# Performance work log

Hardware: AMD Instinct MI355X
Metric: run time of the kernel (lower is better)

## Reference

```python
import jax, jax.numpy as jnp
import numpy as np

B, S, V, H = 64, 512, 128, 1024
TEMP = 1.0


def _lstm_layer(x_seq, W_ih, W_hh, b_ih, b_hh):
    """x_seq: (S, B, D_in) -> (S, B, H). PyTorch gate order: i, f, g, o."""
    Hh = W_hh.shape[1]
    Bb = x_seq.shape[1]
    # precompute input projections for all timesteps: (S, B, 4H)
    xW = jnp.einsum('sbd,gd->sbg', x_seq, W_ih) + (b_ih + b_hh)

    def step(carry, xw_t):
        h, c = carry
        gates = xw_t + h @ W_hh.T  # (B, 4H)
        i, f, g, o = jnp.split(gates, 4, axis=-1)
        i = jax.nn.sigmoid(i)
        f = jax.nn.sigmoid(f)
        g = jnp.tanh(g)
        o = jax.nn.sigmoid(o)
        c = f * c + i * g
        h = o * jnp.tanh(c)
        return (h, c), h

    h0 = jnp.zeros((Bb, Hh), dtype=x_seq.dtype)
    c0 = jnp.zeros((Bb, Hh), dtype=x_seq.dtype)
    _, hs = jax.lax.scan(step, (h0, c0), xW)
    return hs  # (S, B, H)


def setup_inputs() -> dict:
    key = jax.random.key(0)
    ks = jax.random.split(key, 11)
    s = 1.0 / np.sqrt(H)
    u = lambda k, shape: jax.random.uniform(k, shape, jnp.float32, -s, s)
    return {
        'x': jax.random.normal(ks[0], (B, S, V), jnp.float32),
        'W_ih0': u(ks[1], (4 * H, V)),
        'W_hh0': u(ks[2], (4 * H, H)),
        'b_ih0': u(ks[3], (4 * H,)),
        'b_hh0': u(ks[4], (4 * H,)),
        'W_ih1': u(ks[5], (4 * H, H)),
        'W_hh1': u(ks[6], (4 * H, H)),
        'b_ih1': u(ks[7], (4 * H,)),
        'b_hh1': u(ks[8], (4 * H,)),
        'W_fc': u(ks[9], (V, H)),
        'b_fc': u(ks[10], (V,)),
    }


def reference(x, W_ih0, W_hh0, b_ih0, b_hh0, W_ih1, W_hh1, b_ih1, b_hh1, W_fc, b_fc):
    xs = jnp.transpose(x, (1, 0, 2))  # (S, B, V)
    h1 = _lstm_layer(xs, W_ih0, W_hh0, b_ih0, b_hh0)   # (S, B, H)
    h2 = _lstm_layer(h1, W_ih1, W_hh1, b_ih1, b_hh1)   # (S, B, H)
    logits = jnp.einsum('sbh,vh->sbv', h2, W_fc) + b_fc  # (S, B, V)
    out = jax.nn.log_softmax(logits * TEMP, axis=-1)
    return jnp.transpose(out, (1, 0, 2))  # (B, S, V)
```

## Files before the change

kernel.cpp:

```cpp
#include <hip/hip_runtime.h>
#include <hip/hip_bf16.h>
#include <math.h>


#define S_LEN 512
#define B_SZ  64
#define V_SZ  128
#define H_SZ  1024
#define BH    65536
#define RING  8
#define FSTR  16

typedef unsigned short u16;
typedef unsigned short u16x8 __attribute__((ext_vector_type(8)));
typedef __bf16         bf16x8 __attribute__((ext_vector_type(8)));
typedef float          f32x4  __attribute__((ext_vector_type(4)));
typedef int            i32x4  __attribute__((ext_vector_type(4)));

__device__ __forceinline__ u16 f2bf(float f) {
    unsigned int u = __float_as_uint(f);
    u += 0x7fffu + ((u >> 16) & 1u);
    return (u16)(u >> 16);
}
__device__ __forceinline__ f32x4 mfma16(u16x8 a, u16x8 b, f32x4 c) {
    return __builtin_amdgcn_mfma_f32_16x16x32_bf16(
        __builtin_bit_cast(bf16x8, a), __builtin_bit_cast(bf16x8, b), c, 0, 0, 0);
}
__device__ __forceinline__ f32x4 mfma16(i32x4 a, u16x8 b, f32x4 c) {
    return __builtin_amdgcn_mfma_f32_16x16x32_bf16(
        __builtin_bit_cast(bf16x8, a), __builtin_bit_cast(bf16x8, b), c, 0, 0, 0);
}

__device__ __forceinline__ void ld_coh(i32x4& d, const u16* p) {
    asm volatile("global_load_dwordx4 %0, %1, off sc0 sc1" : "=v"(d) : "v"(p));
}
__device__ __forceinline__ void st_coh_u16(u16* p, u16 v) {
    unsigned int vv = v;
    asm volatile("global_store_short %0, %1, off sc0 sc1" :: "v"(p), "v"(vv));
}
__device__ __forceinline__ int ld_flag(const int* p) {
    int v;
    asm volatile("global_load_dword %0, %1, off sc0 sc1\n\ts_waitcnt vmcnt(0)"
                 : "=v"(v) : "v"(p) : "memory");
    return v;
}
__device__ __forceinline__ void st_flag(int* p, int v) {
    asm volatile("global_store_dword %0, %1, off sc0 sc1" :: "v"(p), "v"(v));
}
#define WAITV(n) asm volatile("s_waitcnt vmcnt(" #n ")" ::: "memory")
#define SCHEDB   __builtin_amdgcn_sched_barrier(0)

__global__ __launch_bounds__(256) void cvt_kernel(const float* __restrict__ s,
                                                  u16* __restrict__ d, int n)
{
    int i = (blockIdx.x * 256 + threadIdx.x) * 4;
    if (i >= n) return;
    float4 v = *(const float4*)(s + i);
    ushort4 o;
    o.x = f2bf(v.x); o.y = f2bf(v.y); o.z = f2bf(v.z); o.w = f2bf(v.w);
    *(ushort4*)(d + i) = o;
}

union SMemL {
    struct { u16 wih[64 * 136]; u16 whh[64 * 1032]; } l0;
    struct { u16 w[64 * 1032]; } l1;
    float lg[16][132];
};

__global__ __launch_bounds__(256, 1) void persist_kernel(
    const float* __restrict__ x,
    const u16* __restrict__ Wih0c, const u16* __restrict__ Whh0c,
    const u16* __restrict__ Wih1c, const u16* __restrict__ Whh1c,
    const u16* __restrict__ Wfcc,
    const float* __restrict__ bih0, const float* __restrict__ bhh0,
    const float* __restrict__ bih1, const float* __restrict__ bhh1,
    const float* __restrict__ bfc,
    u16* __restrict__ h0b, u16* __restrict__ h1b,
    int* __restrict__ flagL0, int* __restrict__ flagL1, int* __restrict__ flagFC,
    float* __restrict__ out)
{
    __shared__ SMemL sm;
    const int bid = blockIdx.x, tid = threadIdx.x;
    const int wave = tid >> 6, lane = tid & 63;
    const int l16 = lane & 15, kgi = lane >> 4, kg8 = kgi * 8;

    if (bid < 64) {
        const int j0 = bid * 16, jj = j0 + l16;
        for (int ch = tid; ch < 1024; ch += 256) {
            int rr = ch >> 4, kc = (ch & 15) * 8;
            int gr = (rr >> 4) * H_SZ + j0 + (rr & 15);
            *(u16x8*)&sm.l0.wih[rr * 136 + kc] = *(const u16x8*)(Wih0c + (size_t)gr * V_SZ + kc);
        }
        for (int ch = tid; ch < 8192; ch += 256) {
            int rr = ch >> 7, kc = (ch & 127) * 8;
            int gr = (rr >> 4) * H_SZ + j0 + (rr & 15);
            *(u16x8*)&sm.l0.whh[rr * 1032 + kc] = *(const u16x8*)(Whh0c + (size_t)gr * H_SZ + kc);
        }
        __syncthreads();

        const float bii = bih0[jj]            + bhh0[jj];
        const float bif = bih0[H_SZ + jj]     + bhh0[H_SZ + jj];
        const float big = bih0[2 * H_SZ + jj] + bhh0[2 * H_SZ + jj];
        const float bio = bih0[3 * H_SZ + jj] + bhh0[3 * H_SZ + jj];

        const u16* wihB[4]; const u16* whhB[4];
        #pragma unroll
        for (int g = 0; g < 4; ++g) {
            wihB[g] = &sm.l0.wih[(g * 16 + l16) * 136 + kg8];
            whhB[g] = &sm.l0.whh[(g * 16 + l16) * 1032 + kg8];
        }
        const int arow = wave * 16 + l16;
        const float* xrow = x + (size_t)arow * (S_LEN * V_SZ);
        float creg[4] = {0.f, 0.f, 0.f, 0.f};

        for (int t = 0; t < S_LEN; ++t) {
            {
                const int* p = nullptr; int tgt = 0;
                if (tid < 64)               { p = flagL0 + tid * FSTR;        tgt = t; }
                else if (tid < 192 && t >= 8) { p = flagL1 + (tid - 64) * FSTR; tgt = t - 7; }
                if (p && tgt > 0) while (ld_flag(p) < tgt) __builtin_amdgcn_s_sleep(2);
                __syncthreads();
            }

            f32x4 acc[4][2] = {};
            {
                const float* xp = xrow + (size_t)t * V_SZ + kg8;
                #pragma unroll
                for (int i = 0; i < 4; ++i) {
                    float4 u = *(const float4*)(xp + i * 32);
                    float4 v = *(const float4*)(xp + i * 32 + 4);
                    u16x8 af;
                    af[0] = f2bf(u.x); af[1] = f2bf(u.y); af[2] = f2bf(u.z); af[3] = f2bf(u.w);
                    af[4] = f2bf(v.x); af[5] = f2bf(v.y); af[6] = f2bf(v.z); af[7] = f2bf(v.w);
                    #pragma unroll
                    for (int g = 0; g < 4; ++g)
                        acc[g][i & 1] = mfma16(af, *(const u16x8*)(wihB[g] + i * 32), acc[g][i & 1]);
                }
            }

            {
                auto ISSUE = [&](i32x4 (&buf)[8], const u16* base) {
                    #pragma unroll
                    for (int q = 0; q < 8; ++q) ld_coh(buf[q], base + q * 32);
                };
                auto COMP = [&](i32x4 (&buf)[8], int k0) {
                    #pragma unroll
                    for (int q = 0; q < 8; ++q) {
                        #pragma unroll
                        for (int g = 0; g < 4; ++g)
                            acc[g][q & 1] = mfma16(buf[q],
                                *(const u16x8*)(whhB[g] + (k0 + q) * 32), acc[g][q & 1]);
                    }
                };
                const u16* aB = h0b + (size_t)((t - 1) & 7) * BH + (size_t)arow * H_SZ + kg8;
                i32x4 b0[8], b1[8];
                WAITV(0);
                ISSUE(b0, aB);
                ISSUE(b1, aB + 256); WAITV(8); SCHEDB; COMP(b0, 0);
                ISSUE(b0, aB + 512); WAITV(8); SCHEDB; COMP(b1, 8);
                ISSUE(b1, aB + 768); WAITV(8); SCHEDB; COMP(b0, 16);
                                     WAITV(0); SCHEDB; COMP(b1, 24);
            }

            {
                u16* hout = h0b + (size_t)(t & 7) * BH;
                #pragma unroll
                for (int r = 0; r < 4; ++r) {
                    const int m = wave * 16 + kgi * 4 + r;
                    const float ip = acc[0][0][r] + acc[0][1][r] + bii;
                    const float fp = acc[1][0][r] + acc[1][1][r] + bif;
                    const float gp = acc[2][0][r] + acc[2][1][r] + big;
                    const float op = acc[3][0][r] + acc[3][1][r] + bio;
                    const float iv = 1.f / (1.f + expf(-ip));
                    const float fv = 1.f / (1.f + expf(-fp));
                    const float gv = tanhf(gp);
                    const float ov = 1.f / (1.f + expf(-op));
                    const float cv = fv * creg[r] + iv * gv;
                    creg[r] = cv;
                    st_coh_u16(hout + (size_t)m * H_SZ + jj, f2bf(ov * tanhf(cv)));
                }
                WAITV(0);
            }
            __syncthreads();
            if (tid == 0) st_flag(flagL0 + bid * FSTR, t + 1);
        }
        return;
    }

    if (bid < 192) {
        const int lb = bid - 64, j0 = lb * 8, jj2 = j0 + (l16 & 7);
        for (int ch = tid; ch < 8192; ch += 256) {
            int region = ch >> 12;
            int rl = (ch >> 7) & 31, kc = (ch & 127) * 8;
            int gr = (rl >> 3) * H_SZ + j0 + (rl & 7);
            const u16* src = (region ? Whh1c : Wih1c) + (size_t)gr * H_SZ + kc;
            *(u16x8*)&sm.l1.w[(region * 32 + rl) * 1032 + kc] = *(const u16x8*)src;
        }
        __syncthreads();

        const float bii = bih1[jj2]            + bhh1[jj2];
        const float bif = bih1[H_SZ + jj2]     + bhh1[H_SZ + jj2];
        const float big = bih1[2 * H_SZ + jj2] + bhh1[2 * H_SZ + jj2];
        const float bio = bih1[3 * H_SZ + jj2] + bhh1[3 * H_SZ + jj2];
        const bool lo = (l16 < 8);

        const u16* wB1[2]; const u16* wB2[2];
        #pragma unroll
        for (int nt = 0; nt < 2; ++nt) {
            wB1[nt] = &sm.l1.w[(nt * 16 + l16) * 1032 + kg8];
            wB2[nt] = &sm.l1.w[(32 + nt * 16 + l16) * 1032 + kg8];
        }
        const int arow = wave * 16 + l16;
        float creg[4] = {0.f, 0.f, 0.f, 0.f};

        for (int t = 0; t < S_LEN; ++t) {
            {
                const int* p = nullptr; int tgt = 0;
                if (tid < 64)                     { p = flagL0 + tid * FSTR;         tgt = t + 1; }
                else if (tid < 192)               { p = flagL1 + (tid - 64) * FSTR;  tgt = t; }
                else if (tid < 196 && t >= 8)     { p = flagFC + (tid - 192) * FSTR; tgt = t - 7; }
                if (p && tgt > 0) while (ld_flag(p) < tgt) __builtin_amdgcn_s_sleep(2);
                __syncthreads();
            }

            f32x4 acc[2][2] = {};
            {
                auto ISSUE = [&](i32x4 (&buf)[8], const u16* base) {
                    #pragma unroll
                    for (int q = 0; q < 8; ++q) ld_coh(buf[q], base + q * 32);
                };
                auto COMP = [&](i32x4 (&buf)[8], const u16* const (&wb)[2], int k0) {
                    #pragma unroll
                    for (int q = 0; q < 8; ++q) {
                        #pragma unroll
                        for (int nt = 0; nt < 2; ++nt)
                            acc[nt][q & 1] = mfma16(buf[q],
                                *(const u16x8*)(wb[nt] + (k0 + q) * 32), acc[nt][q & 1]);
                    }
                };
                const u16* a1 = h0b + (size_t)(t & 7) * BH + (size_t)arow * H_SZ + kg8;
                const u16* a2 = h1b + (size_t)((t - 1) & 7) * BH + (size_t)arow * H_SZ + kg8;
                i32x4 b0[8], b1[8];
                WAITV(0);
                ISSUE(b0, a1);
                ISSUE(b1, a1 + 256); WAITV(8); SCHEDB; COMP(b0, wB1, 0);
                ISSUE(b0, a1 + 512); WAITV(8); SCHEDB; COMP(b1, wB1, 8);
                ISSUE(b1, a1 + 768); WAITV(8); SCHEDB; COMP(b0, wB1, 16);
                ISSUE(b0, a2);       WAITV(8); SCHEDB; COMP(b1, wB1, 24);
                ISSUE(b1, a2 + 256); WAITV(8); SCHEDB; COMP(b0, wB2, 0);
                ISSUE(b0, a2 + 512); WAITV(8); SCHEDB; COMP(b1, wB2, 8);
                ISSUE(b1, a2 + 768); WAITV(8); SCHEDB; COMP(b0, wB2, 16);
                                     WAITV(0); SCHEDB; COMP(b1, wB2, 24);
            }

            {
                u16* hout = h1b + (size_t)(t & 7) * BH;
                #pragma unroll
                for (int r = 0; r < 4; ++r) {
                    const float s0 = acc[0][0][r] + acc[0][1][r];
                    const float s1 = acc[1][0][r] + acc[1][1][r];
                    const float q0 = __shfl_xor(s0, 8);
                    const float q1 = __shfl_xor(s1, 8);
                    const float ip = (lo ? s0 : q0) + bii;
                    const float fp = (lo ? q0 : s0) + bif;
                    const float gp = (lo ? s1 : q1) + big;
                    const float op = (lo ? q1 : s1) + bio;
                    const float iv = 1.f / (1.f + expf(-ip));
                    const float fv = 1.f / (1.f + expf(-fp));
                    const float gv = tanhf(gp);
                    const float ov = 1.f / (1.f + expf(-op));
                    const float cv = fv * creg[r] + iv * gv;
                    creg[r] = cv;
                    if (lo) {
                        const int m = wave * 16 + kgi * 4 + r;
                        st_coh_u16(hout + (size_t)m * H_SZ + jj2, f2bf(ov * tanhf(cv)));
                    }
                }
                WAITV(0);
            }
            __syncthreads();
            if (tid == 0) st_flag(flagL1 + lb * FSTR, t + 1);
        }
        return;
    }

    {
        const int fb = bid - 192, m0 = fb * 16;
        const u16* wp[2];
        #pragma unroll
        for (int nt = 0; nt < 2; ++nt)
            wp[nt] = Wfcc + (size_t)(wave * 32 + nt * 16 + l16) * H_SZ + kg8;

        for (int t = 0; t < S_LEN; ++t) {
            {
                const int* p = nullptr; int tgt = 0;
                if (tid < 128) { p = flagL1 + tid * FSTR; tgt = t + 1; }
                if (p && tgt > 0) while (ld_flag(p) < tgt) __builtin_amdgcn_s_sleep(2);
                __syncthreads();
            }

            const u16* aB = h1b + (size_t)(t & 7) * BH + (size_t)(m0 + l16) * H_SZ + kg8;
            f32x4 acc[2][2] = {};
            i32x4 buf[8];
            WAITV(0);
            #pragma unroll
            for (int c = 0; c < 4; ++c) {
                #pragma unroll
                for (int q = 0; q < 8; ++q) ld_coh(buf[q], aB + c * 256 + q * 32);
                WAITV(0); SCHEDB;
                #pragma unroll
                for (int q = 0; q < 8; ++q) {
                    #pragma unroll
                    for (int nt = 0; nt < 2; ++nt)
                        acc[nt][q & 1] = mfma16(buf[q],
                            *(const u16x8*)(wp[nt] + (c * 8 + q) * 32), acc[nt][q & 1]);
                }
            }
            #pragma unroll
            for (int nt = 0; nt < 2; ++nt)
                #pragma unroll
                for (int r = 0; r < 4; ++r) {
                    const int m = kgi * 4 + r, n = wave * 32 + nt * 16 + l16;
                    sm.lg[m][n] = acc[nt][0][r] + acc[nt][1][r] + bfc[n];
                }
            __syncthreads();
            const int row = tid >> 4, sub = tid & 15;
            float vals[8]; float mx = -1e30f;
            #pragma unroll
            for (int q = 0; q < 8; ++q) { vals[q] = sm.lg[row][sub * 8 + q]; mx = fmaxf(mx, vals[q]); }
            #pragma unroll
            for (int o = 1; o < 16; o <<= 1) mx = fmaxf(mx, __shfl_xor(mx, o));
            float se = 0.f;
            #pragma unroll
            for (int q = 0; q < 8; ++q) se += expf(vals[q] - mx);
            #pragma unroll
            for (int o = 1; o < 16; o <<= 1) se += __shfl_xor(se, o);
            const float ls = mx + logf(se);
            float* op = out + (size_t)(m0 + row) * (S_LEN * V_SZ) + (size_t)t * V_SZ + sub * 8;
            #pragma unroll
            for (int q = 0; q < 8; ++q) op[q] = vals[q] - ls;

            __syncthreads();
            if (tid == 0) st_flag(flagFC + fb * FSTR, t + 1);
        }
    }
}

extern "C" void kernel_launch(void* const* d_in, const int* in_sizes, int n_in,
                              void* d_out, int out_size, void* d_ws, size_t ws_size,
                              hipStream_t stream)
{
    const float* x    = (const float*)d_in[0];
    const float* Wih0 = (const float*)d_in[1];
    const float* Whh0 = (const float*)d_in[2];
    const float* bih0 = (const float*)d_in[3];
    const float* bhh0 = (const float*)d_in[4];
    const float* Wih1 = (const float*)d_in[5];
    const float* Whh1 = (const float*)d_in[6];
    const float* bih1 = (const float*)d_in[7];
    const float* bhh1 = (const float*)d_in[8];
    const float* Wfc  = (const float*)d_in[9];
    const float* bfc  = (const float*)d_in[10];
    float* out = (float*)d_out;

    u16* wih0 = (u16*)d_ws;
    u16* whh0 = wih0 + (size_t)4096 * 128;
    u16* wih1 = whh0 + (size_t)4096 * 1024;
    u16* whh1 = wih1 + (size_t)4096 * 1024;
    u16* wfc  = whh1 + (size_t)4096 * 1024;
    u16* h0b  = wfc  + (size_t)128 * 1024;
    u16* h1b  = h0b + (size_t)RING * BH;
    int* flags  = (int*)(h1b + (size_t)RING * BH);
    int* flagL0 = flags;
    int* flagL1 = flagL0 + 64 * FSTR;
    int* flagFC = flagL1 + 128 * FSTR;

    auto cvt = [&](const float* s, u16* d, int n) {
        cvt_kernel<<<(n / 4 + 255) / 256, 256, 0, stream>>>(s, d, n);
    };
    cvt(Wih0, wih0, 4096 * 128);
    cvt(Whh0, whh0, 4096 * 1024);
    cvt(Wih1, wih1, 4096 * 1024);
    cvt(Whh1, whh1, 4096 * 1024);
    cvt(Wfc,  wfc,  128 * 1024);
    hipMemsetAsync(h0b, 0, (size_t)2 * RING * BH * sizeof(u16), stream);
    hipMemsetAsync(flags, 0, (size_t)196 * FSTR * sizeof(int), stream);

    persist_kernel<<<196, 256, 0, stream>>>(
        x, wih0, whh0, wih1, whh1, wfc,
        bih0, bhh0, bih1, bhh1, bfc,
        h0b, h1b, flagL0, flagL1, flagFC, out);
}
```

Measured before the change: 6.229 ms.

## Use non-coherent h loads with a large ring and periodic acquire fences

Replaces the cache-bypassing (sc0 sc1) hidden-state loads with plain global loads. The ring grows to 64 slots with padded slot stride so a stale cached line cannot alias a freshly written slot, and an agent-scope acquire fence every 48 steps invalidates caches. Shared-memory weights are also re-laid out so each lane reads a contiguous 16-byte fragment indexed by lane. The intent is to cut the latency of the per-step recurrent loads. The correctness argument for plain loads depends on cache reuse distance staying within the ring, which is fragile and could read stale data.

```diff
diff --git a/kernel.cpp b/kernel.cpp
--- a/kernel.cpp
+++ b/kernel.cpp
@@ -8,8 +8,10 @@
 #define V_SZ  128
 #define H_SZ  1024
 #define BH    65536
-#define RING  8
+#define RING  64
+#define SLOT  66560
 #define FSTR  16
+#define INVP  48
 
 typedef unsigned short u16;
 typedef unsigned short u16x8 __attribute__((ext_vector_type(8)));
@@ -31,8 +33,8 @@
         __builtin_bit_cast(bf16x8, a), __builtin_bit_cast(bf16x8, b), c, 0, 0, 0);
 }
 
-__device__ __forceinline__ void ld_coh(i32x4& d, const u16* p) {
-    asm volatile("global_load_dwordx4 %0, %1, off sc0 sc1" : "=v"(d) : "v"(p));
+__device__ __forceinline__ void ld_g(i32x4& d, const u16* p) {
+    asm volatile("global_load_dwordx4 %0, %1, off" : "=v"(d) : "v"(p));
 }
 __device__ __forceinline__ void st_coh_u16(u16* p, u16 v) {
     unsigned int vv = v;
@@ -49,6 +51,10 @@
 }
 #define WAITV(n) asm volatile("s_waitcnt vmcnt(" #n ")" ::: "memory")
 #define SCHEDB   __builtin_amdgcn_sched_barrier(0)
+
+__device__ __forceinline__ void l2_acquire_inv() {
+    __builtin_amdgcn_fence(__ATOMIC_ACQUIRE, "agent");
+}
 
 __global__ __launch_bounds__(256) void cvt_kernel(const float* __restrict__ s,
                                                   u16* __restrict__ d, int n)
@@ -62,8 +68,8 @@
 }
 
 union SMemL {
-    struct { u16 wih[64 * 136]; u16 whh[64 * 1032]; } l0;
-    struct { u16 w[64 * 1032]; } l1;
+    struct { u16 wih[4 * 4 * 64 * 8]; u16 whh[32 * 4 * 64 * 8]; } l0;
+    struct { u16 w[2 * 32 * 2 * 64 * 8]; } l1;
     float lg[16][132];
 };
 
@@ -86,15 +92,25 @@
 
     if (bid < 64) {
         const int j0 = bid * 16, jj = j0 + l16;
-        for (int ch = tid; ch < 1024; ch += 256) {
-            int rr = ch >> 4, kc = (ch & 15) * 8;
-            int gr = (rr >> 4) * H_SZ + j0 + (rr & 15);
-            *(u16x8*)&sm.l0.wih[rr * 136 + kc] = *(const u16x8*)(Wih0c + (size_t)gr * V_SZ + kc);
-        }
-        for (int ch = tid; ch < 8192; ch += 256) {
-            int rr = ch >> 7, kc = (ch & 127) * 8;
-            int gr = (rr >> 4) * H_SZ + j0 + (rr & 15);
-            *(u16x8*)&sm.l0.whh[rr * 1032 + kc] = *(const u16x8*)(Whh0c + (size_t)gr * H_SZ + kc);
+        #pragma unroll
+        for (int i = 0; i < 4; ++i) {
+            int f = tid + i * 256;
+            int rl = f >> 4, kf = f & 15;
+            int c = kf >> 2, kg = kf & 3;
+            int g = rl >> 4, jl = rl & 15;
+            int gr = g * H_SZ + j0 + jl;
+            *(u16x8*)&sm.l0.wih[(((c * 4 + g) * 64) + kg * 16 + jl) * 8] =
+                *(const u16x8*)(Wih0c + (size_t)gr * V_SZ + kf * 8);
+        }
+        #pragma unroll
+        for (int i = 0; i < 32; ++i) {
+            int f = tid + i * 256;
+            int rl = f >> 7, kf = f & 127;
+            int c = kf >> 2, kg = kf & 3;
+            int g = rl >> 4, jl = rl & 15;
+            int gr = g * H_SZ + j0 + jl;
+            *(u16x8*)&sm.l0.whh[(((c * 4 + g) * 64) + kg * 16 + jl) * 8] =
+                *(const u16x8*)(Whh0c + (size_t)gr * H_SZ + kf * 8);
         }
         __syncthreads();
 
@@ -103,12 +119,6 @@
         const float big = bih0[2 * H_SZ + jj] + bhh0[2 * H_SZ + jj];
         const float bio = bih0[3 * H_SZ + jj] + bhh0[3 * H_SZ + jj];
 
-        const u16* wihB[4]; const u16* whhB[4];
-        #pragma unroll
-        for (int g = 0; g < 4; ++g) {
-            wihB[g] = &sm.l0.wih[(g * 16 + l16) * 136 + kg8];
-            whhB[g] = &sm.l0.whh[(g * 16 + l16) * 1032 + kg8];
-        }
         const int arow = wave * 16 + l16;
         const float* xrow = x + (size_t)arow * (S_LEN * V_SZ);
         float creg[4] = {0.f, 0.f, 0.f, 0.f};
@@ -116,11 +126,12 @@
         for (int t = 0; t < S_LEN; ++t) {
             {
                 const int* p = nullptr; int tgt = 0;
-                if (tid < 64)               { p = flagL0 + tid * FSTR;        tgt = t; }
-                else if (tid < 192 && t >= 8) { p = flagL1 + (tid - 64) * FSTR; tgt = t - 7; }
+                if (tid < 64)                        { p = flagL0 + tid * FSTR;        tgt = t; }
+                else if (tid < 192 && t >= RING)     { p = flagL1 + (tid - 64) * FSTR; tgt = t - (RING - 1); }
                 if (p && tgt > 0) while (ld_flag(p) < tgt) __builtin_amdgcn_s_sleep(2);
                 __syncthreads();
             }
+            if (t >= INVP && (t % INVP) == 0) l2_acquire_inv();
 
             f32x4 acc[4][2] = {};
             {
@@ -134,14 +145,14 @@
                     af[4] = f2bf(v.x); af[5] = f2bf(v.y); af[6] = f2bf(v.z); af[7] = f2bf(v.w);
                     #pragma unroll
                     for (int g = 0; g < 4; ++g)
-                        acc[g][i & 1] = mfma16(af, *(const u16x8*)(wihB[g] + i * 32), acc[g][i & 1]);
+                        acc[g][i & 1] = mfma16(af,
+                            *(const u16x8*)&sm.l0.wih[((i * 4 + g) * 64 + lane) * 8], acc[g][i & 1]);
                 }
             }
-
             {
                 auto ISSUE = [&](i32x4 (&buf)[8], const u16* base) {
                     #pragma unroll
-                    for (int q = 0; q < 8; ++q) ld_coh(buf[q], base + q * 32);
+                    for (int q = 0; q < 8; ++q) ld_g(buf[q], base + q * 32);
                 };
                 auto COMP = [&](i32x4 (&buf)[8], int k0) {
                     #pragma unroll
@@ -149,10 +160,12 @@
                         #pragma unroll
                         for (int g = 0; g < 4; ++g)
                             acc[g][q & 1] = mfma16(buf[q],
-                                *(const u16x8*)(whhB[g] + (k0 + q) * 32), acc[g][q & 1]);
+                                *(const u16x8*)&sm.l0.whh[(((k0 + q) * 4 + g) * 64 + lane) * 8],
+                                acc[g][q & 1]);
                     }
                 };
-                const u16* aB = h0b + (size_t)((t - 1) & 7) * BH + (size_t)arow * H_SZ + kg8;
+                const u16* aB = h0b + (size_t)((t - 1) & (RING - 1)) * SLOT
+                              + (size_t)arow * H_SZ + kg8;
                 i32x4 b0[8], b1[8];
                 WAITV(0);
                 ISSUE(b0, aB);
@@ -161,9 +174,8 @@
                 ISSUE(b1, aB + 768); WAITV(8); SCHEDB; COMP(b0, 16);
                                      WAITV(0); SCHEDB; COMP(b1, 24);
             }
-
-            {
-                u16* hout = h0b + (size_t)(t & 7) * BH;
+            {
+                u16* hout = h0b + (size_t)(t & (RING - 1)) * SLOT;
                 #pragma unroll
                 for (int r = 0; r < 4; ++r) {
                     const int m = wave * 16 + kgi * 4 + r;
@@ -189,12 +201,18 @@
 
     if (bid < 192) {
         const int lb = bid - 64, j0 = lb * 8, jj2 = j0 + (l16 & 7);
-        for (int ch = tid; ch < 8192; ch += 256) {
-            int region = ch >> 12;
-            int rl = (ch >> 7) & 31, kc = (ch & 127) * 8;
+        #pragma unroll
+        for (int i = 0; i < 32; ++i) {
+            int f = tid + i * 256;
+            int region = f >> 12;
+            int r2 = f & 4095;
+            int rl = r2 >> 7, kf = r2 & 127;
+            int c = kf >> 2, kg = kf & 3;
+            int nt = rl >> 4, jl = rl & 15;
             int gr = (rl >> 3) * H_SZ + j0 + (rl & 7);
-            const u16* src = (region ? Whh1c : Wih1c) + (size_t)gr * H_SZ + kc;
-            *(u16x8*)&sm.l1.w[(region * 32 + rl) * 1032 + kc] = *(const u16x8*)src;
+            const u16* src = (region ? Whh1c : Wih1c) + (size_t)gr * H_SZ + kf * 8;
+            *(u16x8*)&sm.l1.w[((((region * 32 + c) * 2 + nt) * 64) + kg * 16 + jl) * 8] =
+                *(const u16x8*)src;
         }
         __syncthreads();
 
@@ -204,57 +222,54 @@
         const float bio = bih1[3 * H_SZ + jj2] + bhh1[3 * H_SZ + jj2];
         const bool lo = (l16 < 8);
 
-        const u16* wB1[2]; const u16* wB2[2];
-        #pragma unroll
-        for (int nt = 0; nt < 2; ++nt) {
-            wB1[nt] = &sm.l1.w[(nt * 16 + l16) * 1032 + kg8];
-            wB2[nt] = &sm.l1.w[(32 + nt * 16 + l16) * 1032 + kg8];
-        }
         const int arow = wave * 16 + l16;
         float creg[4] = {0.f, 0.f, 0.f, 0.f};
 
         for (int t = 0; t < S_LEN; ++t) {
             {
                 const int* p = nullptr; int tgt = 0;
-                if (tid < 64)                     { p = flagL0 + tid * FSTR;         tgt = t + 1; }
-                else if (tid < 192)               { p = flagL1 + (tid - 64) * FSTR;  tgt = t; }
-                else if (tid < 196 && t >= 8)     { p = flagFC + (tid - 192) * FSTR; tgt = t - 7; }
+                if (tid < 64)                        { p = flagL0 + tid * FSTR;         tgt = t + 1; }
+                else if (tid < 192)                  { p = flagL1 + (tid - 64) * FSTR;  tgt = t; }
+                else if (tid < 196 && t >= RING)     { p = flagFC + (tid - 192) * FSTR; tgt = t - (RING - 1); }
                 if (p && tgt > 0) while (ld_flag(p) < tgt) __builtin_amdgcn_s_sleep(2);
                 __syncthreads();
             }
+            if (t >= INVP && (t % INVP) == 0) l2_acquire_inv();
 
             f32x4 acc[2][2] = {};
             {
                 auto ISSUE = [&](i32x4 (&buf)[8], const u16* base) {
                     #pragma unroll
-                    for (int q = 0; q < 8; ++q) ld_coh(buf[q], base + q * 32);
+                    for (int q = 0; q < 8; ++q) ld_g(buf[q], base + q * 32);
                 };
-                auto COMP = [&](i32x4 (&buf)[8], const u16* const (&wb)[2], int k0) {
+                auto COMP = [&](i32x4 (&buf)[8], int region, int c0) {
                     #pragma unroll
                     for (int q = 0; q < 8; ++q) {
                         #pragma unroll
                         for (int nt = 0; nt < 2; ++nt)
                             acc[nt][q & 1] = mfma16(buf[q],
-                                *(const u16x8*)(wb[nt] + (k0 + q) * 32), acc[nt][q & 1]);
+                                *(const u16x8*)&sm.l1.w[(((region * 32 + c0 + q) * 2 + nt) * 64 + lane) * 8],
+                                acc[nt][q & 1]);
                     }
                 };
-                const u16* a1 = h0b + (size_t)(t & 7) * BH + (size_t)arow * H_SZ + kg8;
-                const u16* a2 = h1b + (size_t)((t - 1) & 7) * BH + (size_t)arow * H_SZ + kg8;
+                const u16* a1 = h0b + (size_t)(t & (RING - 1)) * SLOT
+                              + (size_t)arow * H_SZ + kg8;
+                const u16* a2 = h1b + (size_t)((t - 1) & (RING - 1)) * SLOT
+                              + (size_t)arow * H_SZ + kg8;
                 i32x4 b0[8], b1[8];
                 WAITV(0);
                 ISSUE(b0, a1);
-                ISSUE(b1, a1 + 256); WAITV(8); SCHEDB; COMP(b0, wB1, 0);
-                ISSUE(b0, a1 + 512); WAITV(8); SCHEDB; COMP(b1, wB1, 8);
-                ISSUE(b1, a1 + 768); WAITV(8); SCHEDB; COMP(b0, wB1, 16);
-                ISSUE(b0, a2);       WAITV(8); SCHEDB; COMP(b1, wB1, 24);
-                ISSUE(b1, a2 + 256); WAITV(8); SCHEDB; COMP(b0, wB2, 0);
-                ISSUE(b0, a2 + 512); WAITV(8); SCHEDB; COMP(b1, wB2, 8);
-                ISSUE(b1, a2 + 768); WAITV(8); SCHEDB; COMP(b0, wB2, 16);
-                                     WAITV(0); SCHEDB; COMP(b1, wB2, 24);
-            }
-
-            {
-                u16* hout = h1b + (size_t)(t & 7) * BH;
+                ISSUE(b1, a1 + 256); WAITV(8); SCHEDB; COMP(b0, 0, 0);
+                ISSUE(b0, a1 + 512); WAITV(8); SCHEDB; COMP(b1, 0, 8);
+                ISSUE(b1, a1 + 768); WAITV(8); SCHEDB; COMP(b0, 0, 16);
+                ISSUE(b0, a2);       WAITV(8); SCHEDB; COMP(b1, 0, 24);
+                ISSUE(b1, a2 + 256); WAITV(8); SCHEDB; COMP(b0, 1, 0);
+                ISSUE(b0, a2 + 512); WAITV(8); SCHEDB; COMP(b1, 1, 8);
+                ISSUE(b1, a2 + 768); WAITV(8); SCHEDB; COMP(b0, 1, 16);
+                                     WAITV(0); SCHEDB; COMP(b1, 1, 24);
+            }
+            {
+                u16* hout = h1b + (size_t)(t & (RING - 1)) * SLOT;
                 #pragma unroll
                 for (int r = 0; r < 4; ++r) {
                     const float s0 = acc[0][0][r] + acc[0][1][r];
@@ -298,15 +313,17 @@
                 if (p && tgt > 0) while (ld_flag(p) < tgt) __builtin_amdgcn_s_sleep(2);
                 __syncthreads();
             }
-
-            const u16* aB = h1b + (size_t)(t & 7) * BH + (size_t)(m0 + l16) * H_SZ + kg8;
+            if (t >= INVP && (t % INVP) == 0) l2_acquire_inv();
+
+            const u16* aB = h1b + (size_t)(t & (RING - 1)) * SLOT
+                          + (size_t)(m0 + l16) * H_SZ + kg8;
             f32x4 acc[2][2] = {};
             i32x4 buf[8];
             WAITV(0);
             #pragma unroll
             for (int c = 0; c < 4; ++c) {
                 #pragma unroll
-                for (int q = 0; q < 8; ++q) ld_coh(buf[q], aB + c * 256 + q * 32);
+                for (int q = 0; q < 8; ++q) ld_g(buf[q], aB + c * 256 + q * 32);
                 WAITV(0); SCHEDB;
                 #pragma unroll
                 for (int q = 0; q < 8; ++q) {
@@ -369,8 +386,8 @@
     u16* whh1 = wih1 + (size_t)4096 * 1024;
     u16* wfc  = whh1 + (size_t)4096 * 1024;
     u16* h0b  = wfc  + (size_t)128 * 1024;
-    u16* h1b  = h0b + (size_t)RING * BH;
-    int* flags  = (int*)(h1b + (size_t)RING * BH);
+    u16* h1b  = h0b + (size_t)RING * SLOT;
+    int* flags  = (int*)(h1b + (size_t)RING * SLOT);
     int* flagL0 = flags;
     int* flagL1 = flagL0 + 64 * FSTR;
     int* flagFC = flagL1 + 128 * FSTR;
@@ -383,7 +400,8 @@
     cvt(Wih1, wih1, 4096 * 1024);
     cvt(Whh1, whh1, 4096 * 1024);
     cvt(Wfc,  wfc,  128 * 1024);
-    hipMemsetAsync(h0b, 0, (size_t)2 * RING * BH * sizeof(u16), stream);
+    hipMemsetAsync(h0b + (size_t)(RING - 1) * SLOT, 0, (size_t)BH * sizeof(u16), stream);
+    hipMemsetAsync(h1b + (size_t)(RING - 1) * SLOT, 0, (size_t)BH * sizeof(u16), stream);
     hipMemsetAsync(flags, 0, (size_t)196 * FSTR * sizeof(int), stream);
 
     persist_kernel<<<196, 256, 0, stream>>>(
```

New measurement: 6.553 ms. 1.05x slower.
